# Optimization experiments

Hardware: AMD Instinct MI355X
Metric: run time of the kernel (lower is better)

Reference implementation:

```python
import jax, jax.numpy as jnp
import numpy as np

BATCH = 8192
IN_FEATURES = 1024
OUT_FEATURES = 1024
GRID_SIZE = 5
SPLINE_ORDER = 3
GRID_MIN, GRID_MAX = -1.0, 1.0
NUM_BASES = GRID_SIZE + SPLINE_ORDER  # 8
GRID_LEN = GRID_SIZE + 2 * SPLINE_ORDER + 1  # 12


def setup_inputs() -> dict:
    key = jax.random.key(0)
    k1, k2, k3 = jax.random.split(key, 3)
    x = jax.random.normal(k1, (BATCH, IN_FEATURES), dtype=jnp.float32)
    base_weight = jax.random.normal(k2, (OUT_FEATURES, IN_FEATURES), dtype=jnp.float32) * 0.1
    spline_weight = jax.random.normal(k3, (OUT_FEATURES, IN_FEATURES, NUM_BASES), dtype=jnp.float32) * 0.1
    grid = jnp.linspace(GRID_MIN, GRID_MAX, GRID_LEN, dtype=jnp.float32)  # buffer, not learned
    return {"x": x, "base_weight": base_weight, "spline_weight": spline_weight, "grid": grid}


def _bspline_basis(xc, grid, order):
    """Iterative Cox-de Boor DP, vectorized over all features and basis indices.
    xc: [B, F] clamped inputs; grid: [G] uniform knots (all denominators > 0).
    Returns [B, F, G - order - 1] = [B, F, NUM_BASES]."""
    G = grid.shape[0]
    xe = xc[..., None]  # [B, F, 1]
    # k = 0: indicator of knot interval, matches (x >= grid[i]) & (x < grid[i+1])
    B = ((xe >= grid[:-1]) & (xe < grid[1:])).astype(xc.dtype)  # [B, F, G-1]
    for k in range(1, order + 1):
        left = (xe - grid[: G - k - 1]) / (grid[k : G - 1] - grid[: G - k - 1]) * B[..., :-1]
        right = (grid[k + 1 : G] - xe) / (grid[k + 1 : G] - grid[1 : G - k]) * B[..., 1:]
        B = left + right  # [B, F, G-1-k]
    return B


def reference(x, base_weight, spline_weight, grid):
    # base path: SiLU activation then linear
    base_output = jax.nn.silu(x) @ base_weight.T  # [B, out]
    # spline path: B-spline basis per feature, weighted sum over (in, basis)
    x_clamped = jnp.clip(x, GRID_MIN * 0.99, GRID_MAX * 0.99)
    basis = _bspline_basis(x_clamped, grid, SPLINE_ORDER)  # [B, in, NUM_BASES]
    spline_output = jnp.einsum("bin,oin->bo", basis, spline_weight)
    return base_output + spline_output
```

## Files before the change

### kernel.cpp

```cpp
#include <hip/hip_runtime.h>
#include <stdint.h>

typedef _Float16 f16;
typedef __attribute__((ext_vector_type(8))) _Float16 f16x8;
typedef __attribute__((ext_vector_type(4))) float f32x4;

#define BATCH 8192
#define INF   1024
#define OUTF  1024
#define KTOT  9216
#define NT    72
#define CONV_BLOCKS 4608

__device__ __forceinline__ void gload16(const void* g, void* l) {
  __builtin_amdgcn_global_load_lds(
      (const __attribute__((address_space(1))) uint32_t*)g,
      (__attribute__((address_space(3))) uint32_t*)l, 16, 0, 0);
}

__global__ __launch_bounds__(256) void fused_prep_kernel(
    const float* __restrict__ bw, const float* __restrict__ sw,
    const float* __restrict__ x, const float* __restrict__ grid,
    f16* __restrict__ Wb, f16* __restrict__ Abuf)
{
  int blk = blockIdx.x;
  if (blk < CONV_BLOCKS) {
    int idx = blk * 256 + threadIdx.x;
    int o = idx / 1152;
    int r = idx - o * 1152;
    int k8 = r * 8;
    const float* src = (k8 < INF) ? (bw + (size_t)o * INF + k8)
                                  : (sw + (size_t)o * (INF * 8) + (k8 - INF));
    float4 v0 = *(const float4*)src;
    float4 v1 = *(const float4*)(src + 4);
    f16x8 ov;
    ov[0] = (f16)v0.x; ov[1] = (f16)v0.y; ov[2] = (f16)v0.z; ov[3] = (f16)v0.w;
    ov[4] = (f16)v1.x; ov[5] = (f16)v1.y; ov[6] = (f16)v1.z; ov[7] = (f16)v1.w;
    *(f16x8*)(Wb + (size_t)o * KTOT + k8) = ov;
    return;
  }

  int q = (blk - CONV_BLOCKS) * 256 + threadIdx.x;
  int b = q >> 8;
  int i0 = (q & 255) << 2;
  float4 xv = *(const float4*)(x + ((size_t)b << 10) + i0);
  float xa[4] = {xv.x, xv.y, xv.z, xv.w};

  float g[12];
#pragma unroll
  for (int j = 0; j < 12; ++j) g[j] = grid[j];
  float H  = g[1] - g[0];
  float r1 = 1.0f / H;
  float r2 = 0.5f * r1;
  float r3 = (1.0f / 3.0f) * r1;

  f16 sil[4];
  f16x8 bas[4];
#pragma unroll
  for (int e = 0; e < 4; ++e) {
    float v = xa[e];
    sil[e] = (f16)(v / (1.0f + __expf(-v)));
    float xe = fminf(fmaxf(v, -0.99f), 0.99f);
    float Bv[11];
#pragma unroll
    for (int j = 0; j < 11; ++j) Bv[j] = (xe >= g[j] && xe < g[j + 1]) ? 1.0f : 0.0f;
#pragma unroll
    for (int j = 0; j < 10; ++j) Bv[j] = (xe - g[j]) * r1 * Bv[j] + (g[j + 2] - xe) * r1 * Bv[j + 1];
#pragma unroll
    for (int j = 0; j < 9; ++j)  Bv[j] = (xe - g[j]) * r2 * Bv[j] + (g[j + 3] - xe) * r2 * Bv[j + 1];
#pragma unroll
    for (int j = 0; j < 8; ++j)  Bv[j] = (xe - g[j]) * r3 * Bv[j] + (g[j + 4] - xe) * r3 * Bv[j + 1];
#pragma unroll
    for (int n = 0; n < 8; ++n) bas[e][n] = (f16)Bv[n];
  }
  f16* row = Abuf + (size_t)b * KTOT;
  *(uint64_t*)(row + i0) = *(const uint64_t*)sil;
  f16* bp = row + INF + (size_t)i0 * 8;
#pragma unroll
  for (int e = 0; e < 4; ++e) *(f16x8*)(bp + e * 8) = bas[e];
}

#define LDA(base, m, s) (*(const f16x8*)((base) + ((wr*128 + (m)*16 + la) * 64 + ((((s)*4 + lb) ^ lasw) * 8))))
#define LDB(base, n, s) (*(const f16x8*)((base) + ((wcn*64 + (n)*16 + la) * 64 + ((((s)*4 + lb) ^ lasw) * 8))))

#define MFMA1(m, n, s) acc[m][n] = __builtin_amdgcn_mfma_f32_16x16x32_f16(af[m][s], bf[n][s], acc[m][n], 0, 0, 0)
#define MFMA_S0(m0) do { \
  MFMA1(m0,0,0);   MFMA1(m0,1,0);   MFMA1(m0,2,0);   MFMA1(m0,3,0); \
  MFMA1(m0+1,0,0); MFMA1(m0+1,1,0); MFMA1(m0+1,2,0); MFMA1(m0+1,3,0); } while (0)
#define MFMA_S1(m0) do { \
  MFMA1(m0,0,1);   MFMA1(m0,1,1);   MFMA1(m0,2,1);   MFMA1(m0,3,1); \
  MFMA1(m0+1,0,1); MFMA1(m0+1,1,1); MFMA1(m0+1,2,1); MFMA1(m0+1,3,1); } while (0)

#define SCHED0 __builtin_amdgcn_sched_barrier(0)
#define SBARF do { __builtin_amdgcn_s_barrier(); SCHED0; } while (0)

template <bool ATOMIC>
__global__ __launch_bounds__(512, 2) void kan_gemm_kernel(
    const f16* __restrict__ A, const f16* __restrict__ W,
    float* __restrict__ C, float* __restrict__ P1)
{
  __shared__ __align__(16) f16 lsA[2 * 256 * 64];
  __shared__ __align__(16) f16 lsB[2 * 256 * 64];

  const size_t K = KTOT;
  int bid = blockIdx.x;
  int xcd = bid & 7;
  int u   = bid >> 3;
  int tm  = xcd * 4 + (u & 3);
  int tn  = (u >> 2) & 3;
  int split = u >> 4;
  size_t kbase = (size_t)split * (NT * 64);

  int tid = threadIdx.x;
  int w = tid >> 6, l = tid & 63;
  int wr = w >> 2, wcn = w & 3;
  int la = l & 15, lb = l >> 4, lasw = la & 7;

  int rh = tid >> 3;
  int sc = (tid & 7) ^ (rh & 7);
  const f16* aSrc0 = A + (size_t)(tm * 256 + rh) * K + kbase + sc * 8;
  const f16* bSrc0 = W + (size_t)(tn * 256 + rh) * K + kbase + sc * 8;

  auto stage = [&](int h) {
    if (h >= 4 * NT) return;
    int tile = h >> 2, ty = h & 3, half = ty & 1;
    size_t koff = (size_t)tile * 64;
    if (ty < 2) {
      const f16* s = aSrc0 + (size_t)half * 128 * K + koff;
      f16* d = lsA + (tile & 1) * 16384 + half * 8192 + w * 512;
      gload16(s, d);
      gload16(s + 64 * K, d + 4096);
    } else {
      const f16* s = bSrc0 + (size_t)half * 128 * K + koff;
      f16* d = lsB + (tile & 1) * 16384 + half * 8192 + w * 512;
      gload16(s, d);
      gload16(s + 64 * K, d + 4096);
    }
  };

  f16x8 af[8][2], bf[4][2];
  f32x4 acc[8][4] = {};

  stage(2); stage(3); stage(0); stage(1); stage(6); stage(7);
  asm volatile("s_waitcnt vmcnt(4)" ::: "memory");
  SBARF;
  {
    const f16* bA = lsA; const f16* bB = lsB;
#pragma unroll
    for (int n = 0; n < 4; ++n) bf[n][0] = LDB(bB, n, 0);
    af[0][0] = LDA(bA, 0, 0); af[0][1] = LDA(bA, 0, 1);
    af[1][0] = LDA(bA, 1, 0); af[1][1] = LDA(bA, 1, 1);
  }

  for (int t = 0; t < NT; ++t) {
    const f16* bA  = lsA + (t & 1) * 16384;
    const f16* bB  = lsB + (t & 1) * 16384;
    const f16* bA1 = lsA + ((t + 1) & 1) * 16384;
    const f16* bB1 = lsB + ((t + 1) & 1) * 16384;
    int h1 = 4 * (t + 1), h2 = 4 * (t + 2);

    stage(h1 + 0); stage(h1 + 1);
    SBARF;
    __builtin_amdgcn_s_setprio(1);
    bf[0][1] = LDB(bB, 0, 1); bf[1][1] = LDB(bB, 1, 1);
    bf[2][1] = LDB(bB, 2, 1); bf[3][1] = LDB(bB, 3, 1);
    af[2][0] = LDA(bA, 2, 0); af[3][0] = LDA(bA, 3, 0);
    MFMA_S0(0);
    af[2][1] = LDA(bA, 2, 1); af[3][1] = LDA(bA, 3, 1);
    MFMA_S1(0);
    __builtin_amdgcn_s_setprio(0);
    SBARF;

    stage(h2 + 2);
    SBARF;
    __builtin_amdgcn_s_setprio(1);
    af[4][0] = LDA(bA, 4, 0); af[5][0] = LDA(bA, 5, 0);
    MFMA_S0(2);
    af[4][1] = LDA(bA, 4, 1); af[5][1] = LDA(bA, 5, 1);
    MFMA_S1(2);
    __builtin_amdgcn_s_setprio(0);
    SBARF;

    stage(h2 + 3);
    SBARF;
    __builtin_amdgcn_s_setprio(1);
    af[6][0] = LDA(bA, 6, 0); af[7][0] = LDA(bA, 7, 0);
    MFMA_S0(4);
    af[6][1] = LDA(bA, 6, 1); af[7][1] = LDA(bA, 7, 1);
    MFMA_S1(4);
    __builtin_amdgcn_s_setprio(0);
    SBARF;

    if (t < NT - 2)       asm volatile("s_waitcnt vmcnt(4)" ::: "memory");
    else if (t == NT - 2) asm volatile("s_waitcnt vmcnt(0)" ::: "memory");
    SBARF;
    __builtin_amdgcn_s_setprio(1);
    MFMA_S0(6);
    if (t < NT - 1) {
      bf[0][0] = LDB(bB1, 0, 0); bf[1][0] = LDB(bB1, 1, 0);
      bf[2][0] = LDB(bB1, 2, 0); bf[3][0] = LDB(bB1, 3, 0);
      af[0][0] = LDA(bA1, 0, 0); af[0][1] = LDA(bA1, 0, 1);
      af[1][0] = LDA(bA1, 1, 0); af[1][1] = LDA(bA1, 1, 1);
    }
    MFMA_S1(6);
    __builtin_amdgcn_s_setprio(0);
    SBARF;
  }

  int rowBase = tm * 256 + wr * 128 + lb * 4;
  int colBase = tn * 256 + wcn * 64 + la;
  float* dst = ATOMIC ? C : (split ? P1 : C);
#pragma unroll
  for (int m = 0; m < 8; ++m)
#pragma unroll
    for (int n = 0; n < 4; ++n) {
      int col = colBase + n * 16;
#pragma unroll
      for (int j = 0; j < 4; ++j) {
        int row = rowBase + m * 16 + j;
        if (ATOMIC) atomicAdd(&C[(size_t)row * OUTF + col], acc[m][n][j]);
        else        dst[(size_t)row * OUTF + col] = acc[m][n][j];
      }
    }
}

__global__ __launch_bounds__(256) void reduce_kernel(
    float* __restrict__ out, const float* __restrict__ p)
{
  size_t i = ((size_t)blockIdx.x * 256 + threadIdx.x) * 4;
  f32x4 a = *(f32x4*)(out + i);
  f32x4 b = *(const f32x4*)(p + i);
  a += b;
  *(f32x4*)(out + i) = a;
}

extern "C" void kernel_launch(void* const* d_in, const int* in_sizes, int n_in,
                              void* d_out, int out_size, void* d_ws, size_t ws_size,
                              hipStream_t stream)
{
  const float* x  = (const float*)d_in[0];
  const float* bw = (const float*)d_in[1];
  const float* sw = (const float*)d_in[2];
  const float* gr = (const float*)d_in[3];
  float* out = (float*)d_out;

  f16* Wb = (f16*)d_ws;
  size_t wBytes = (size_t)OUTF * KTOT * sizeof(f16);
  f16* Abuf = (f16*)((char*)d_ws + wBytes);
  size_t aBytes = (size_t)BATCH * KTOT * sizeof(f16);
  size_t oBytes = (size_t)BATCH * OUTF * sizeof(float);

  int prepBlocks = (BATCH * INF / 4) / 256;
  fused_prep_kernel<<<CONV_BLOCKS + prepBlocks, 256, 0, stream>>>(
      bw, sw, x, gr, Wb, Abuf);

  if (ws_size >= wBytes + aBytes + oBytes) {
    float* P1 = (float*)((char*)d_ws + wBytes + aBytes);
    kan_gemm_kernel<false><<<256, 512, 0, stream>>>(Abuf, Wb, out, P1);
    reduce_kernel<<<(int)(oBytes / sizeof(float) / 4 / 256), 256, 0, stream>>>(out, P1);
  } else {
    hipMemsetAsync(d_out, 0, oBytes, stream);
    kan_gemm_kernel<true><<<256, 512, 0, stream>>>(Abuf, Wb, out, nullptr);
  }
}
```

Measured before the change: 203.7 us.

## Simplify GEMM main loop to single-barrier double-buffer pipeline

Replaces the multi-phase main loop (four barrier-separated sub-phases with staggered global-to-LDS stages and register prefetch of the next tile) with a simpler schedule. Each iteration now issues all four stages for the next tile up front, runs all LDS reads and MFMAs for the current tile, then waits for all loads and synchronizes once. This cuts barrier count and the vmcnt bookkeeping per tile. In exchange it loses cross-iteration register prefetch and leaves a single outstanding tile of global loads, which may expose more latency.

```diff
diff --git a/kernel.cpp b/kernel.cpp
--- a/kernel.cpp
+++ b/kernel.cpp
@@ -141,70 +141,42 @@
   f16x8 af[8][2], bf[4][2];
   f32x4 acc[8][4] = {};
 
-  stage(2); stage(3); stage(0); stage(1); stage(6); stage(7);
-  asm volatile("s_waitcnt vmcnt(4)" ::: "memory");
-  SBARF;
-  {
-    const f16* bA = lsA; const f16* bB = lsB;
-#pragma unroll
-    for (int n = 0; n < 4; ++n) bf[n][0] = LDB(bB, n, 0);
-    af[0][0] = LDA(bA, 0, 0); af[0][1] = LDA(bA, 0, 1);
-    af[1][0] = LDA(bA, 1, 0); af[1][1] = LDA(bA, 1, 1);
-  }
+  stage(0); stage(1); stage(2); stage(3);
+  asm volatile("s_waitcnt vmcnt(0)" ::: "memory");
+  SCHED0;
 
   for (int t = 0; t < NT; ++t) {
-    const f16* bA  = lsA + (t & 1) * 16384;
-    const f16* bB  = lsB + (t & 1) * 16384;
-    const f16* bA1 = lsA + ((t + 1) & 1) * 16384;
-    const f16* bB1 = lsB + ((t + 1) & 1) * 16384;
-    int h1 = 4 * (t + 1), h2 = 4 * (t + 2);
-
+    const f16* bA = lsA + (t & 1) * 16384;
+    const f16* bB = lsB + (t & 1) * 16384;
+    int h1 = 4 * (t + 1);
+
+    SBARF;
     stage(h1 + 0); stage(h1 + 1);
-    SBARF;
+    stage(h1 + 2); stage(h1 + 3);
     __builtin_amdgcn_s_setprio(1);
+    af[0][0] = LDA(bA, 0, 0); af[1][0] = LDA(bA, 1, 0);
+    bf[0][0] = LDB(bB, 0, 0); bf[1][0] = LDB(bB, 1, 0);
+    bf[2][0] = LDB(bB, 2, 0); bf[3][0] = LDB(bB, 3, 0);
+    af[0][1] = LDA(bA, 0, 1); af[1][1] = LDA(bA, 1, 1);
     bf[0][1] = LDB(bB, 0, 1); bf[1][1] = LDB(bB, 1, 1);
     bf[2][1] = LDB(bB, 2, 1); bf[3][1] = LDB(bB, 3, 1);
     af[2][0] = LDA(bA, 2, 0); af[3][0] = LDA(bA, 3, 0);
     MFMA_S0(0);
     af[2][1] = LDA(bA, 2, 1); af[3][1] = LDA(bA, 3, 1);
     MFMA_S1(0);
-    __builtin_amdgcn_s_setprio(0);
-    SBARF;
-
-    stage(h2 + 2);
-    SBARF;
-    __builtin_amdgcn_s_setprio(1);
     af[4][0] = LDA(bA, 4, 0); af[5][0] = LDA(bA, 5, 0);
     MFMA_S0(2);
     af[4][1] = LDA(bA, 4, 1); af[5][1] = LDA(bA, 5, 1);
     MFMA_S1(2);
-    __builtin_amdgcn_s_setprio(0);
-    SBARF;
-
-    stage(h2 + 3);
-    SBARF;
-    __builtin_amdgcn_s_setprio(1);
     af[6][0] = LDA(bA, 6, 0); af[7][0] = LDA(bA, 7, 0);
     MFMA_S0(4);
     af[6][1] = LDA(bA, 6, 1); af[7][1] = LDA(bA, 7, 1);
     MFMA_S1(4);
-    __builtin_amdgcn_s_setprio(0);
-    SBARF;
-
-    if (t < NT - 2)       asm volatile("s_waitcnt vmcnt(4)" ::: "memory");
-    else if (t == NT - 2) asm volatile("s_waitcnt vmcnt(0)" ::: "memory");
-    SBARF;
-    __builtin_amdgcn_s_setprio(1);
     MFMA_S0(6);
-    if (t < NT - 1) {
-      bf[0][0] = LDB(bB1, 0, 0); bf[1][0] = LDB(bB1, 1, 0);
-      bf[2][0] = LDB(bB1, 2, 0); bf[3][0] = LDB(bB1, 3, 0);
-      af[0][0] = LDA(bA1, 0, 0); af[0][1] = LDA(bA1, 0, 1);
-      af[1][0] = LDA(bA1, 1, 0); af[1][1] = LDA(bA1, 1, 1);
-    }
     MFMA_S1(6);
     __builtin_amdgcn_s_setprio(0);
-    SBARF;
+    asm volatile("s_waitcnt vmcnt(0)" ::: "memory");
+    SCHED0;
   }
 
   int rowBase = tm * 256 + wr * 128 + lb * 4;
```

Measured after the change: 227.9 us. 1.12x slower.
